# Kernel tuning notes

Hardware: AMD Instinct MI355X
Metric: run time of the kernel (lower is better)

Reference implementation:

```python
import jax, jax.numpy as jnp
import numpy as np

D_MODEL = 1024
N_HEADS = 16
D_V = D_MODEL // N_HEADS  # 64; o_proj maps d_model -> d_v (quirk of the source)
B, S = 4, 2048


def setup_inputs() -> dict:
    key = jax.random.key(0)
    ks = jax.random.split(key, 5)
    scale = 1.0 / np.sqrt(D_MODEL)
    return {
        "in_features": jax.random.normal(ks[0], (B, S, D_MODEL), dtype=jnp.float32),
        "Wq": jax.random.normal(ks[1], (D_MODEL, D_MODEL), dtype=jnp.float32) * scale,
        "Wk": jax.random.normal(ks[2], (D_MODEL, D_MODEL), dtype=jnp.float32) * scale,
        "Wv": jax.random.normal(ks[3], (D_MODEL, D_MODEL), dtype=jnp.float32) * scale,
        "Wo": jax.random.normal(ks[4], (D_V, D_MODEL), dtype=jnp.float32) * scale,
    }


def reference(in_features, Wq, Wk, Wv, Wo):
    # Linear(in, out): y = x @ W^T, no bias. NOTE: source never splits heads;
    # attention runs single-head over the full d_model dims.
    Q = jnp.einsum('bsd,ed->bse', in_features, Wq)  # [B,S,D]
    K = jnp.einsum('bsd,ed->bse', in_features, Wk)
    V = jnp.einsum('bsd,ed->bse', in_features, Wv)

    scores = jnp.einsum('bqd,bkd->bqk', Q, K)       # [B,S,S]
    causal = jnp.tril(jnp.ones((S, S), dtype=bool))  # True = keep
    # source applies -inf mask BEFORE scaling (equivalent result)
    scores = jnp.where(causal[None, :, :], scores, -jnp.inf)
    scores = scores / jnp.sqrt(jnp.float32(D_MODEL))  # K.size(-1) == d_model
    attn = jax.nn.softmax(scores, axis=-1)
    ctx = jnp.einsum('bqk,bkd->bqd', attn, V)        # [B,S,D]
    return jnp.einsum('bsd,vd->bsv', ctx, Wo)        # [B,S,D_V]
```

## Files before the change

kernel.cpp:

```cpp
#include <hip/hip_runtime.h>
#include <math.h>

typedef unsigned short u16;
typedef unsigned int u32;
typedef __attribute__((ext_vector_type(8))) short short8;
typedef __attribute__((ext_vector_type(4))) short short4v;
typedef __attribute__((ext_vector_type(4))) float f32x4;

#define BB 4
#define SS 2048
#define DD 1024
#define DV 64
#define NYU 1152
#define BS (BB * SS)
#define SCALE (1.0f / 32.0f)

__device__ __forceinline__ u16 f2bf(float f) {
    u32 u = __builtin_bit_cast(u32, f);
    u32 r = u + 0x7fffu + ((u >> 16) & 1u);
    return (u16)(r >> 16);
}
__device__ __forceinline__ float bf2f(u16 b) {
    return __builtin_bit_cast(float, (u32)b << 16);
}
__device__ __forceinline__ void storeC(float* p, float v) { *p = v; }
__device__ __forceinline__ void storeC(u16* p, float v) { *p = f2bf(v); }

__global__ __launch_bounds__(256) void prep(const float* __restrict__ x,
                                            const float* __restrict__ Wq,
                                            const float* __restrict__ Wk,
                                            const float* __restrict__ Wo,
                                            const float* __restrict__ Wv,
                                            u16* __restrict__ x16,
                                            u16* __restrict__ Wqt,
                                            u16* __restrict__ Wkt,
                                            float* __restrict__ wpart,
                                            float* __restrict__ out,
                                            float* __restrict__ Lacc) {
    __shared__ float smem[64 * 128];
    const int b = blockIdx.x;
    const int tid = threadIdx.x;
    if (b < 8192) {
        int i = b * 256 + tid;
        f32x4 v = ((const f32x4*)x)[i];
        short4v o;
        o.x = (short)f2bf(v.x); o.y = (short)f2bf(v.y);
        o.z = (short)f2bf(v.z); o.w = (short)f2bf(v.w);
        ((short4v*)x16)[i] = o;
    } else if (b < 8704) {
        const int bb = b - 8192;
        const float* src = (bb >> 8) ? Wk : Wq;
        u16* dst = (bb >> 8) ? Wkt : Wqt;
        const int rem = bb & 255;
        const int e0 = (rem >> 4) * 64, d0 = (rem & 15) * 64;
        u16* t = (u16*)smem;
        const int g = tid >> 6, lane = tid & 63;
        for (int r = g; r < 64; r += 4)
            t[r * 72 + lane] = f2bf(src[(size_t)(e0 + r) * DD + d0 + lane]);
        __syncthreads();
        for (int r = g; r < 64; r += 4)
            dst[(size_t)(d0 + r) * DD + e0 + lane] = t[lane * 72 + r];
    } else if (b < 8768) {
        const int bb = b - 8704;
        const int echunk = (bb & 7) * 128;
        const int kc = bb >> 3, kbase = kc * 128;
        for (int idx = tid; idx < 64 * 128; idx += 256)
            smem[idx] = Wo[(size_t)(idx >> 7) * DD + kbase + (idx & 127)];
        __syncthreads();
        const int eo = echunk + (tid & 31) * 4;
        const int ob = (tid >> 5) * 8;
        float acc[8][4] = {};
        for (int k = 0; k < 128; ++k) {
            f32x4 wv = *(const f32x4*)&Wv[(size_t)(kbase + k) * DD + eo];
#pragma unroll
            for (int oi = 0; oi < 8; ++oi) {
                float s = smem[(ob + oi) * 128 + k];
                acc[oi][0] += s * wv.x; acc[oi][1] += s * wv.y;
                acc[oi][2] += s * wv.z; acc[oi][3] += s * wv.w;
            }
        }
#pragma unroll
        for (int oi = 0; oi < 8; ++oi)
            *(f32x4*)&wpart[((size_t)kc * 64 + ob + oi) * DD + eo] =
                (f32x4){acc[oi][0], acc[oi][1], acc[oi][2], acc[oi][3]};
    } else if (b < 9280) {
        int i = (b - 8768) * 256 + tid;
        ((f32x4*)out)[i] = (f32x4){0.f, 0.f, 0.f, 0.f};
    } else {
        int i = (b - 9280) * 256 + tid;
        ((f32x4*)Lacc)[i] = (f32x4){0.f, 0.f, 0.f, 0.f};
    }
}

__global__ __launch_bounds__(256) void reduce_all(const float* __restrict__ Gpart,
                                                  const float* __restrict__ wpart,
                                                  u16* __restrict__ Wall2) {
    const int bx = blockIdx.x;
    const int e0 = threadIdx.x * 4;
    f32x4 s = (f32x4){0.f, 0.f, 0.f, 0.f};
    if (bx < 1024) {
#pragma unroll
        for (int kc = 0; kc < 4; ++kc)
            s += *(const f32x4*)&Gpart[(size_t)kc * DD * DD + (size_t)bx * DD + e0];
    } else {
#pragma unroll
        for (int kc = 0; kc < 8; ++kc)
            s += *(const f32x4*)&wpart[((size_t)kc * 64 + bx - 1024) * DD + e0];
    }
    short4v ov;
    ov.x = (short)f2bf(s.x); ov.y = (short)f2bf(s.y);
    ov.z = (short)f2bf(s.z); ov.w = (short)f2bf(s.w);
    *(short4v*)&Wall2[(size_t)bx * DD + e0] = ov;
}

template <int TM, int TN, int WM, int WN, typename OutT, int MODE>
__global__ __launch_bounds__(WM * WN * 64) void gemm_nt_mfma(
    const u16* __restrict__ A, const u16* __restrict__ B, OutT* __restrict__ C,
    int lda, int ldb, int ldc, int K, long sA, long sB, long sC,
    u16* __restrict__ Utp) {
    constexpr int NW = WM * WN;
    constexpr int CA = TM / 16;
    constexpr int CB = TN / 16;

    const int z = blockIdx.z;
    A += (size_t)z * sA;
    B += (size_t)z * sB;
    C += (size_t)z * sC;
    int m0, n0;
    if constexpr (MODE == 3) {
        const int b = blockIdx.x;
        const int r = b & 7, q = b >> 3;
        m0 = (r * 8 + q / 9) * TM;
        n0 = (q % 9) * TN;
    } else {
        m0 = blockIdx.y * TM;
        n0 = blockIdx.x * TN;
    }

    __shared__ u16 As[2][TM * 32];
    __shared__ u16 Bs[2][TN * 32];

    const int tid = threadIdx.x;
    const int w = tid >> 6, lane = tid & 63;
    const int wm = w / WN, wn = w % WN;
    const int lrow = lane >> 2;
    const int lcolsw = (((lane & 3) ^ ((lrow >> 1) & 3)) << 3);
    const int m16 = lane & 15;
    const int khg = lane >> 4;
    const int rdo = ((khg ^ ((m16 >> 1) & 3)) << 3);

    f32x4 acc[4][4];
#pragma unroll
    for (int i = 0; i < 4; ++i)
#pragma unroll
        for (int j = 0; j < 4; ++j) acc[i][j] = (f32x4){0.f, 0.f, 0.f, 0.f};

    auto stage = [&](int t, int bufi) {
        const int k0 = t * 32;
        for (int c = w; c < CA; c += NW) {
            const u16* g = A + (size_t)(m0 + c * 16 + lrow) * lda + k0 + lcolsw;
            __builtin_amdgcn_global_load_lds(
                (const __attribute__((address_space(1))) void*)g,
                (__attribute__((address_space(3))) void*)(&As[bufi][c * 512]), 16, 0, 0);
        }
        for (int c = w; c < CB; c += NW) {
            const u16* g = B + (size_t)(n0 + c * 16 + lrow) * ldb + k0 + lcolsw;
            __builtin_amdgcn_global_load_lds(
                (const __attribute__((address_space(1))) void*)g,
                (__attribute__((address_space(3))) void*)(&Bs[bufi][c * 512]), 16, 0, 0);
        }
    };

    const int nk = K >> 5;
    stage(0, 0);
    int cur = 0;
    for (int t = 0; t < nk; ++t) {
        asm volatile("s_waitcnt vmcnt(0)" ::: "memory");
        __syncthreads();
        if (t + 1 < nk) stage(t + 1, cur ^ 1);

        short8 a[4], b[4];
#pragma unroll
        for (int i = 0; i < 4; ++i)
            a[i] = *(const short8*)&As[cur][(wm * 64 + i * 16 + m16) * 32 + rdo];
#pragma unroll
        for (int j = 0; j < 4; ++j)
            b[j] = *(const short8*)&Bs[cur][(wn * 64 + j * 16 + m16) * 32 + rdo];
#pragma unroll
        for (int i = 0; i < 4; ++i)
#pragma unroll
            for (int j = 0; j < 4; ++j)
                acc[i][j] = __builtin_amdgcn_mfma_f32_16x16x32_bf16(a[i], b[j], acc[i][j], 0, 0, 0);
        cur ^= 1;
    }

    const int crow0 = m0 + wm * 64 + (lane >> 4) * 4;
    const int ccol0 = n0 + wn * 64 + m16;
#pragma unroll
    for (int i = 0; i < 4; ++i)
#pragma unroll
        for (int j = 0; j < 4; ++j)
#pragma unroll
            for (int r = 0; r < 4; ++r) {
                const float v = acc[i][j][r];
                storeC(&C[(size_t)(crow0 + i * 16 + r) * ldc + ccol0 + j * 16], v);
                if constexpr (MODE == 3) {
                    if (n0 == 1024 && wn == 0)
                        Utp[(size_t)(ccol0 + j * 16 - 1024) * BS + crow0 + i * 16 + r] = f2bf(v);
                }
            }
}

__global__ __launch_bounds__(256) void scores_pv(const u16* __restrict__ YU,
                                                 const u16* __restrict__ x16,
                                                 const u16* __restrict__ Ut,
                                                 float* __restrict__ out,
                                                 float* __restrict__ Lacc) {
    const int b = blockIdx.x;
    const int r8 = b & 7;
    const int z = r8 >> 1;
    const int t = 2 * (b >> 3) + (r8 & 1);
    int y = (int)((sqrtf(8.f * t + 1.f) - 1.f) * 0.5f);
    while ((y + 1) * (y + 2) / 2 <= t) ++y;
    while (y * (y + 1) / 2 > t) --y;
    const int m0 = y * 128;
    const int n0 = (t - y * (y + 1) / 2) * 128;

    const u16* A = YU + (size_t)z * SS * NYU;
    const u16* B = x16 + (size_t)z * SS * DD;

    __shared__ union ShU {
        struct { u16 As[2][128 * 32]; u16 Bs[2][128 * 32]; } s;
        u16 Ps[128 * 136];
    } sh;

    const int tid = threadIdx.x;
    const int w = tid >> 6, lane = tid & 63;
    const int wm = w >> 1, wn = w & 1;
    const int lrow = lane >> 2;
    const int lcolsw = (((lane & 3) ^ ((lrow >> 1) & 3)) << 3);
    const int m16 = lane & 15;
    const int kh = (lane >> 4) * 8;
    const int rdo = (((lane >> 4) ^ ((m16 >> 1) & 3)) << 3);

    f32x4 acc[4][4];
#pragma unroll
    for (int i = 0; i < 4; ++i)
#pragma unroll
        for (int j = 0; j < 4; ++j) acc[i][j] = (f32x4){0.f, 0.f, 0.f, 0.f};

    auto stage = [&](int tt, int bufi) {
        const int k0 = tt * 32;
        for (int c = w; c < 8; c += 4) {
            const u16* g = A + (size_t)(m0 + c * 16 + lrow) * NYU + k0 + lcolsw;
            __builtin_amdgcn_global_load_lds(
                (const __attribute__((address_space(1))) void*)g,
                (__attribute__((address_space(3))) void*)(&sh.s.As[bufi][c * 512]), 16, 0, 0);
        }
        for (int c = w; c < 8; c += 4) {
            const u16* g = B + (size_t)(n0 + c * 16 + lrow) * DD + k0 + lcolsw;
            __builtin_amdgcn_global_load_lds(
                (const __attribute__((address_space(1))) void*)g,
                (__attribute__((address_space(3))) void*)(&sh.s.Bs[bufi][c * 512]), 16, 0, 0);
        }
    };

    stage(0, 0);
    int cur = 0;
    for (int tt = 0; tt < 32; ++tt) {
        asm volatile("s_waitcnt vmcnt(0)" ::: "memory");
        __syncthreads();
        if (tt + 1 < 32) stage(tt + 1, cur ^ 1);

        short8 a[4], bb[4];
#pragma unroll
        for (int i = 0; i < 4; ++i)
            a[i] = *(const short8*)&sh.s.As[cur][(wm * 64 + i * 16 + m16) * 32 + rdo];
#pragma unroll
        for (int j = 0; j < 4; ++j)
            bb[j] = *(const short8*)&sh.s.Bs[cur][(wn * 64 + j * 16 + m16) * 32 + rdo];
#pragma unroll
        for (int i = 0; i < 4; ++i)
#pragma unroll
            for (int j = 0; j < 4; ++j)
                acc[i][j] = __builtin_amdgcn_mfma_f32_16x16x32_bf16(a[i], bb[j], acc[i][j], 0, 0, 0);
        cur ^= 1;
    }
    __syncthreads();

    const int rl0 = wm * 64 + (lane >> 4) * 4;
    const int cl0 = wn * 64 + m16;
#pragma unroll
    for (int i = 0; i < 4; ++i)
#pragma unroll
        for (int j = 0; j < 4; ++j)
#pragma unroll
            for (int r = 0; r < 4; ++r) {
                const int rl = rl0 + i * 16 + r;
                const int cl = cl0 + j * 16;
                float p = __expf(acc[i][j][r] * SCALE);
                sh.Ps[rl * 136 + cl] = (n0 + cl <= m0 + rl) ? f2bf(p) : (u16)0;
            }
    __syncthreads();

    short8 ones8;
#pragma unroll
    for (int e = 0; e < 8; ++e) ones8[e] = (short)0x3F80;

    const u16* Utz = Ut + (size_t)z * SS + n0;
    f32x4 accO[2][4], accL[2];
#pragma unroll
    for (int i = 0; i < 2; ++i) {
        accL[i] = (f32x4){0.f, 0.f, 0.f, 0.f};
#pragma unroll
        for (int j = 0; j < 4; ++j) accO[i][j] = (f32x4){0.f, 0.f, 0.f, 0.f};
    }
#pragma unroll
    for (int ks = 0; ks < 4; ++ks) {
        const int k0 = ks * 32;
        short8 a[2], bb[4];
#pragma unroll
        for (int i = 0; i < 2; ++i)
            a[i] = *(const short8*)&sh.Ps[(w * 32 + i * 16 + m16) * 136 + k0 + kh];
#pragma unroll
        for (int j = 0; j < 4; ++j)
            bb[j] = *(const short8*)&Utz[(size_t)(j * 16 + m16) * BS + k0 + kh];
#pragma unroll
        for (int i = 0; i < 2; ++i) {
#pragma unroll
            for (int j = 0; j < 4; ++j)
                accO[i][j] = __builtin_amdgcn_mfma_f32_16x16x32_bf16(a[i], bb[j], accO[i][j], 0, 0, 0);
            accL[i] = __builtin_amdgcn_mfma_f32_16x16x32_bf16(a[i], ones8, accL[i], 0, 0, 0);
        }
    }

    float* Oz = out + (size_t)z * SS * DV;
    float* Lz = Lacc + (size_t)z * SS;
    const int wrow = m0 + w * 32 + (lane >> 4) * 4;
#pragma unroll
    for (int i = 0; i < 2; ++i) {
#pragma unroll
        for (int j = 0; j < 4; ++j)
#pragma unroll
            for (int r = 0; r < 4; ++r)
                atomicAdd(&Oz[(size_t)(wrow + i * 16 + r) * DV + j * 16 + m16],
                          accO[i][j][r]);
        if (m16 == 0)
#pragma unroll
            for (int r = 0; r < 4; ++r)
                atomicAdd(&Lz[wrow + i * 16 + r], accL[i][r]);
    }
}

__global__ __launch_bounds__(256) void normalize(float* __restrict__ out,
                                                 const float* __restrict__ Lacc) {
    int i = blockIdx.x * 256 + threadIdx.x;
    f32x4 v = ((f32x4*)out)[i];
    const float inv = 1.f / Lacc[(i * 4) >> 6];
    v.x *= inv; v.y *= inv; v.z *= inv; v.w *= inv;
    ((f32x4*)out)[i] = v;
}

extern "C" void kernel_launch(void* const* d_in, const int* in_sizes, int n_in,
                              void* d_out, int out_size, void* d_ws, size_t ws_size,
                              hipStream_t stream) {
    const float* x  = (const float*)d_in[0];
    const float* Wq = (const float*)d_in[1];
    const float* Wk = (const float*)d_in[2];
    const float* Wv = (const float*)d_in[3];
    const float* Wo = (const float*)d_in[4];
    float* out = (float*)d_out;

    u16* x16   = (u16*)d_ws;
    u16* Wqt16 = x16 + (size_t)BB * SS * DD;
    u16* Wkt16 = Wqt16 + (size_t)DD * DD;
    u16* Wall2 = Wkt16 + (size_t)DD * DD;
    u16* YU    = Wall2 + (size_t)NYU * DD;
    u16* Ut    = YU + (size_t)BB * SS * NYU;
    float* wpart = (float*)(Ut + (size_t)DV * BS);
    float* Lacc  = wpart + (size_t)8 * 64 * DD;
    float* Gpart = (float*)YU;

    prep<<<dim3(9288), 256, 0, stream>>>(x, Wq, Wk, Wo, Wv, x16, Wqt16, Wkt16,
                                         wpart, out, Lacc);

    gemm_nt_mfma<128, 128, 2, 2, float, 0><<<dim3(8, 8, 4), 256, 0, stream>>>(
        Wkt16, Wqt16, Gpart, DD, DD, DD, 256, 256, 256, (long)DD * DD, nullptr);

    reduce_all<<<dim3(1088), 256, 0, stream>>>(Gpart, wpart, Wall2);

    gemm_nt_mfma<128, 128, 2, 2, u16, 3><<<dim3(576), 256, 0, stream>>>(
        x16, Wall2, YU, DD, DD, NYU, DD, 0, 0, 0, Ut);

    scores_pv<<<dim3(544), 256, 0, stream>>>(YU, x16, Ut, out, Lacc);

    normalize<<<dim3(out_size / 4 / 256), 256, 0, stream>>>(out, Lacc);
}
```

Before: 200.2 us.

## Triple-buffer GEMM K-loop with partial vmcnt waits and smaller Gram tiles

The GEMM and scores kernels move from double to triple buffering in LDS. Loads for tile t+2 are issued before computing tile t, and the wait only drains older loads (vmcnt(LPT)), leaving one barrier per iteration. The GEMM template is generalized to any tile size, and the Wq/Wk Gram GEMM moves to 64x64 tiles to launch more blocks. The prep kernel is also reordered so the long Wv·Wo blocks are scheduled first. This raises LDS usage, which may lower occupancy, and the scores kernel's union grows to fit three buffers.

```diff
diff --git a/kernel.cpp b/kernel.cpp
--- a/kernel.cpp
+++ b/kernel.cpp
@@ -25,6 +25,17 @@
 }
 __device__ __forceinline__ void storeC(float* p, float v) { *p = v; }
 __device__ __forceinline__ void storeC(u16* p, float v) { *p = f2bf(v); }
+
+template <int N>
+__device__ __forceinline__ void wait_vm() {
+    if constexpr (N == 0) asm volatile("s_waitcnt vmcnt(0)" ::: "memory");
+    else if constexpr (N == 1) asm volatile("s_waitcnt vmcnt(1)" ::: "memory");
+    else if constexpr (N == 2) asm volatile("s_waitcnt vmcnt(2)" ::: "memory");
+    else if constexpr (N == 3) asm volatile("s_waitcnt vmcnt(3)" ::: "memory");
+    else if constexpr (N == 4) asm volatile("s_waitcnt vmcnt(4)" ::: "memory");
+    else if constexpr (N == 6) asm volatile("s_waitcnt vmcnt(6)" ::: "memory");
+    else if constexpr (N == 8) asm volatile("s_waitcnt vmcnt(8)" ::: "memory");
+}
 
 __global__ __launch_bounds__(256) void prep(const float* __restrict__ x,
                                             const float* __restrict__ Wq,
@@ -40,15 +51,31 @@
     __shared__ float smem[64 * 128];
     const int b = blockIdx.x;
     const int tid = threadIdx.x;
-    if (b < 8192) {
-        int i = b * 256 + tid;
-        f32x4 v = ((const f32x4*)x)[i];
-        short4v o;
-        o.x = (short)f2bf(v.x); o.y = (short)f2bf(v.y);
-        o.z = (short)f2bf(v.z); o.w = (short)f2bf(v.w);
-        ((short4v*)x16)[i] = o;
-    } else if (b < 8704) {
-        const int bb = b - 8192;
+    if (b < 64) {
+        const int bb = b;
+        const int echunk = (bb & 7) * 128;
+        const int kc = bb >> 3, kbase = kc * 128;
+        for (int idx = tid; idx < 64 * 128; idx += 256)
+            smem[idx] = Wo[(size_t)(idx >> 7) * DD + kbase + (idx & 127)];
+        __syncthreads();
+        const int eo = echunk + (tid & 31) * 4;
+        const int ob = (tid >> 5) * 8;
+        float acc[8][4] = {};
+        for (int k = 0; k < 128; ++k) {
+            f32x4 wv = *(const f32x4*)&Wv[(size_t)(kbase + k) * DD + eo];
+#pragma unroll
+            for (int oi = 0; oi < 8; ++oi) {
+                float s = smem[(ob + oi) * 128 + k];
+                acc[oi][0] += s * wv.x; acc[oi][1] += s * wv.y;
+                acc[oi][2] += s * wv.z; acc[oi][3] += s * wv.w;
+            }
+        }
+#pragma unroll
+        for (int oi = 0; oi < 8; ++oi)
+            *(f32x4*)&wpart[((size_t)kc * 64 + ob + oi) * DD + eo] =
+                (f32x4){acc[oi][0], acc[oi][1], acc[oi][2], acc[oi][3]};
+    } else if (b < 576) {
+        const int bb = b - 64;
         const float* src = (bb >> 8) ? Wk : Wq;
         u16* dst = (bb >> 8) ? Wkt : Wqt;
         const int rem = bb & 255;
@@ -61,28 +88,12 @@
         for (int r = g; r < 64; r += 4)
             dst[(size_t)(d0 + r) * DD + e0 + lane] = t[lane * 72 + r];
     } else if (b < 8768) {
-        const int bb = b - 8704;
-        const int echunk = (bb & 7) * 128;
-        const int kc = bb >> 3, kbase = kc * 128;
-        for (int idx = tid; idx < 64 * 128; idx += 256)
-            smem[idx] = Wo[(size_t)(idx >> 7) * DD + kbase + (idx & 127)];
-        __syncthreads();
-        const int eo = echunk + (tid & 31) * 4;
-        const int ob = (tid >> 5) * 8;
-        float acc[8][4] = {};
-        for (int k = 0; k < 128; ++k) {
-            f32x4 wv = *(const f32x4*)&Wv[(size_t)(kbase + k) * DD + eo];
-#pragma unroll
-            for (int oi = 0; oi < 8; ++oi) {
-                float s = smem[(ob + oi) * 128 + k];
-                acc[oi][0] += s * wv.x; acc[oi][1] += s * wv.y;
-                acc[oi][2] += s * wv.z; acc[oi][3] += s * wv.w;
-            }
-        }
-#pragma unroll
-        for (int oi = 0; oi < 8; ++oi)
-            *(f32x4*)&wpart[((size_t)kc * 64 + ob + oi) * DD + eo] =
-                (f32x4){acc[oi][0], acc[oi][1], acc[oi][2], acc[oi][3]};
+        int i = (b - 576) * 256 + tid;
+        f32x4 v = ((const f32x4*)x)[i];
+        short4v o;
+        o.x = (short)f2bf(v.x); o.y = (short)f2bf(v.y);
+        o.z = (short)f2bf(v.z); o.w = (short)f2bf(v.w);
+        ((short4v*)x16)[i] = o;
     } else if (b < 9280) {
         int i = (b - 8768) * 256 + tid;
         ((f32x4*)out)[i] = (f32x4){0.f, 0.f, 0.f, 0.f};
@@ -121,6 +132,11 @@
     constexpr int NW = WM * WN;
     constexpr int CA = TM / 16;
     constexpr int CB = TN / 16;
+    constexpr int RT = TM / WM;
+    constexpr int CT = TN / WN;
+    constexpr int AI = RT / 16;
+    constexpr int AJ = CT / 16;
+    constexpr int LPT = CA / NW + CB / NW;
 
     const int z = blockIdx.z;
     A += (size_t)z * sA;
@@ -130,15 +146,16 @@
     if constexpr (MODE == 3) {
         const int b = blockIdx.x;
         const int r = b & 7, q = b >> 3;
-        m0 = (r * 8 + q / 9) * TM;
+        constexpr int RPX = 8192 / TM / 8;
+        m0 = (r * RPX + q / 9) * TM;
         n0 = (q % 9) * TN;
     } else {
         m0 = blockIdx.y * TM;
         n0 = blockIdx.x * TN;
     }
 
-    __shared__ u16 As[2][TM * 32];
-    __shared__ u16 Bs[2][TN * 32];
+    __shared__ u16 As[3][TM * 32];
+    __shared__ u16 Bs[3][TN * 32];
 
     const int tid = threadIdx.x;
     const int w = tid >> 6, lane = tid & 63;
@@ -146,14 +163,13 @@
     const int lrow = lane >> 2;
     const int lcolsw = (((lane & 3) ^ ((lrow >> 1) & 3)) << 3);
     const int m16 = lane & 15;
-    const int khg = lane >> 4;
-    const int rdo = ((khg ^ ((m16 >> 1) & 3)) << 3);
-
-    f32x4 acc[4][4];
-#pragma unroll
-    for (int i = 0; i < 4; ++i)
-#pragma unroll
-        for (int j = 0; j < 4; ++j) acc[i][j] = (f32x4){0.f, 0.f, 0.f, 0.f};
+    const int rdo = (((lane >> 4) ^ ((m16 >> 1) & 3)) << 3);
+
+    f32x4 acc[AI][AJ];
+#pragma unroll
+    for (int i = 0; i < AI; ++i)
+#pragma unroll
+        for (int j = 0; j < AJ; ++j) acc[i][j] = (f32x4){0.f, 0.f, 0.f, 0.f};
 
     auto stage = [&](int t, int bufi) {
         const int k0 = t * 32;
@@ -173,33 +189,38 @@
 
     const int nk = K >> 5;
     stage(0, 0);
-    int cur = 0;
+    if (nk > 1) { stage(1, 1); wait_vm<LPT>(); } else { wait_vm<0>(); }
+    __syncthreads();
+
+    int rb = 0, sb = 2;
     for (int t = 0; t < nk; ++t) {
-        asm volatile("s_waitcnt vmcnt(0)" ::: "memory");
-        __syncthreads();
-        if (t + 1 < nk) stage(t + 1, cur ^ 1);
-
-        short8 a[4], b[4];
-#pragma unroll
-        for (int i = 0; i < 4; ++i)
-            a[i] = *(const short8*)&As[cur][(wm * 64 + i * 16 + m16) * 32 + rdo];
-#pragma unroll
-        for (int j = 0; j < 4; ++j)
-            b[j] = *(const short8*)&Bs[cur][(wn * 64 + j * 16 + m16) * 32 + rdo];
-#pragma unroll
-        for (int i = 0; i < 4; ++i)
-#pragma unroll
-            for (int j = 0; j < 4; ++j)
+        if (t + 2 < nk) stage(t + 2, sb);
+
+        short8 a[AI], b[AJ];
+#pragma unroll
+        for (int i = 0; i < AI; ++i)
+            a[i] = *(const short8*)&As[rb][(wm * RT + i * 16 + m16) * 32 + rdo];
+#pragma unroll
+        for (int j = 0; j < AJ; ++j)
+            b[j] = *(const short8*)&Bs[rb][(wn * CT + j * 16 + m16) * 32 + rdo];
+#pragma unroll
+        for (int i = 0; i < AI; ++i)
+#pragma unroll
+            for (int j = 0; j < AJ; ++j)
                 acc[i][j] = __builtin_amdgcn_mfma_f32_16x16x32_bf16(a[i], b[j], acc[i][j], 0, 0, 0);
-        cur ^= 1;
-    }
-
-    const int crow0 = m0 + wm * 64 + (lane >> 4) * 4;
-    const int ccol0 = n0 + wn * 64 + m16;
-#pragma unroll
-    for (int i = 0; i < 4; ++i)
-#pragma unroll
-        for (int j = 0; j < 4; ++j)
+
+        if (t + 2 < nk) { wait_vm<LPT>(); __syncthreads(); }
+        else if (t + 1 < nk) { wait_vm<0>(); __syncthreads(); }
+        rb = (rb == 2) ? 0 : rb + 1;
+        sb = (sb == 2) ? 0 : sb + 1;
+    }
+
+    const int crow0 = m0 + wm * RT + (lane >> 4) * 4;
+    const int ccol0 = n0 + wn * CT + m16;
+#pragma unroll
+    for (int i = 0; i < AI; ++i)
+#pragma unroll
+        for (int j = 0; j < AJ; ++j)
 #pragma unroll
             for (int r = 0; r < 4; ++r) {
                 const float v = acc[i][j][r];
@@ -230,7 +251,7 @@
     const u16* B = x16 + (size_t)z * SS * DD;
 
     __shared__ union ShU {
-        struct { u16 As[2][128 * 32]; u16 Bs[2][128 * 32]; } s;
+        struct { u16 As[3][128 * 32]; u16 Bs[3][128 * 32]; } s;
         u16 Ps[128 * 136];
     } sh;
 
@@ -266,25 +287,31 @@
     };
 
     stage(0, 0);
-    int cur = 0;
+    stage(1, 1);
+    wait_vm<4>();
+    __syncthreads();
+
+    int rb = 0, sb = 2;
     for (int tt = 0; tt < 32; ++tt) {
-        asm volatile("s_waitcnt vmcnt(0)" ::: "memory");
-        __syncthreads();
-        if (tt + 1 < 32) stage(tt + 1, cur ^ 1);
+        if (tt + 2 < 32) stage(tt + 2, sb);
 
         short8 a[4], bb[4];
 #pragma unroll
         for (int i = 0; i < 4; ++i)
-            a[i] = *(const short8*)&sh.s.As[cur][(wm * 64 + i * 16 + m16) * 32 + rdo];
+            a[i] = *(const short8*)&sh.s.As[rb][(wm * 64 + i * 16 + m16) * 32 + rdo];
 #pragma unroll
         for (int j = 0; j < 4; ++j)
-            bb[j] = *(const short8*)&sh.s.Bs[cur][(wn * 64 + j * 16 + m16) * 32 + rdo];
+            bb[j] = *(const short8*)&sh.s.Bs[rb][(wn * 64 + j * 16 + m16) * 32 + rdo];
 #pragma unroll
         for (int i = 0; i < 4; ++i)
 #pragma unroll
             for (int j = 0; j < 4; ++j)
                 acc[i][j] = __builtin_amdgcn_mfma_f32_16x16x32_bf16(a[i], bb[j], acc[i][j], 0, 0, 0);
-        cur ^= 1;
+
+        if (tt + 2 < 32) { wait_vm<4>(); __syncthreads(); }
+        else if (tt + 1 < 32) { wait_vm<0>(); __syncthreads(); }
+        rb = (rb == 2) ? 0 : rb + 1;
+        sb = (sb == 2) ? 0 : sb + 1;
     }
     __syncthreads();
 
@@ -384,7 +411,7 @@
     prep<<<dim3(9288), 256, 0, stream>>>(x, Wq, Wk, Wo, Wv, x16, Wqt16, Wkt16,
                                          wpart, out, Lacc);
 
-    gemm_nt_mfma<128, 128, 2, 2, float, 0><<<dim3(8, 8, 4), 256, 0, stream>>>(
+    gemm_nt_mfma<64, 64, 2, 2, float, 0><<<dim3(16, 16, 4), 256, 0, stream>>>(
         Wkt16, Wqt16, Gpart, DD, DD, DD, 256, 256, 256, (long)DD * DD, nullptr);
 
     reduce_all<<<dim3(1088), 256, 0, stream>>>(Gpart, wpart, Wall2);
```

New measurement: 193.1 us. 3.6% less time.

## Replace atomics with per-tile partials, MFMA weight products, restructure GEMM pipeline sync

Applied to the files above, without the earlier changes.

scores_pv now writes each tile's partial output and row-sum into its own slot, and normalize reduces those slots per row. This removes the fp32 atomicAdds and the zero-fill passes over out and Lacc. The Wo·Wv product moves from a scalar fp32 loop in prep to a bf16 MFMA kernel that also computes the split-K Wk^T·Wq Gram partials in 64x64 tiles. Partials are stored in bf16, which halves reduce traffic but loses some precision. The double-buffered GEMM loops now issue the next stage before waiting, giving slightly more load/compute overlap, and the template GEMM is split into specialized kernels.

```diff
diff --git a/kernel.cpp b/kernel.cpp
--- a/kernel.cpp
+++ b/kernel.cpp
@@ -14,6 +14,8 @@
 #define NYU 1152
 #define BS (BB * SS)
 #define SCALE (1.0f / 32.0f)
+#define NTILE 136
+#define NSLOT (BB * NTILE)
 
 __device__ __forceinline__ u16 f2bf(float f) {
     u32 u = __builtin_bit_cast(u32, f);
@@ -23,131 +25,191 @@
 __device__ __forceinline__ float bf2f(u16 b) {
     return __builtin_bit_cast(float, (u32)b << 16);
 }
-__device__ __forceinline__ void storeC(float* p, float v) { *p = v; }
-__device__ __forceinline__ void storeC(u16* p, float v) { *p = f2bf(v); }
 
 __global__ __launch_bounds__(256) void prep(const float* __restrict__ x,
                                             const float* __restrict__ Wq,
                                             const float* __restrict__ Wk,
+                                            const float* __restrict__ Wv,
                                             const float* __restrict__ Wo,
-                                            const float* __restrict__ Wv,
                                             u16* __restrict__ x16,
                                             u16* __restrict__ Wqt,
                                             u16* __restrict__ Wkt,
-                                            float* __restrict__ wpart,
-                                            float* __restrict__ out,
-                                            float* __restrict__ Lacc) {
-    __shared__ float smem[64 * 128];
+                                            u16* __restrict__ Wvt,
+                                            u16* __restrict__ Wo16) {
+    __shared__ u16 t[64 * 72];
     const int b = blockIdx.x;
     const int tid = threadIdx.x;
-    if (b < 8192) {
-        int i = b * 256 + tid;
-        f32x4 v = ((const f32x4*)x)[i];
-        short4v o;
-        o.x = (short)f2bf(v.x); o.y = (short)f2bf(v.y);
-        o.z = (short)f2bf(v.z); o.w = (short)f2bf(v.w);
-        ((short4v*)x16)[i] = o;
-    } else if (b < 8704) {
-        const int bb = b - 8192;
-        const float* src = (bb >> 8) ? Wk : Wq;
-        u16* dst = (bb >> 8) ? Wkt : Wqt;
-        const int rem = bb & 255;
+    if (b < 768) {
+        const int sel = b >> 8;
+        const float* src = (sel == 0) ? Wq : (sel == 1) ? Wk : Wv;
+        u16* dst = (sel == 0) ? Wqt : (sel == 1) ? Wkt : Wvt;
+        const int rem = b & 255;
         const int e0 = (rem >> 4) * 64, d0 = (rem & 15) * 64;
-        u16* t = (u16*)smem;
         const int g = tid >> 6, lane = tid & 63;
         for (int r = g; r < 64; r += 4)
             t[r * 72 + lane] = f2bf(src[(size_t)(e0 + r) * DD + d0 + lane]);
         __syncthreads();
         for (int r = g; r < 64; r += 4)
             dst[(size_t)(d0 + r) * DD + e0 + lane] = t[lane * 72 + r];
-    } else if (b < 8768) {
-        const int bb = b - 8704;
-        const int echunk = (bb & 7) * 128;
-        const int kc = bb >> 3, kbase = kc * 128;
-        for (int idx = tid; idx < 64 * 128; idx += 256)
-            smem[idx] = Wo[(size_t)(idx >> 7) * DD + kbase + (idx & 127)];
-        __syncthreads();
-        const int eo = echunk + (tid & 31) * 4;
-        const int ob = (tid >> 5) * 8;
-        float acc[8][4] = {};
-        for (int k = 0; k < 128; ++k) {
-            f32x4 wv = *(const f32x4*)&Wv[(size_t)(kbase + k) * DD + eo];
-#pragma unroll
-            for (int oi = 0; oi < 8; ++oi) {
-                float s = smem[(ob + oi) * 128 + k];
-                acc[oi][0] += s * wv.x; acc[oi][1] += s * wv.y;
-                acc[oi][2] += s * wv.z; acc[oi][3] += s * wv.w;
-            }
-        }
-#pragma unroll
-        for (int oi = 0; oi < 8; ++oi)
-            *(f32x4*)&wpart[((size_t)kc * 64 + ob + oi) * DD + eo] =
-                (f32x4){acc[oi][0], acc[oi][1], acc[oi][2], acc[oi][3]};
-    } else if (b < 9280) {
-        int i = (b - 8768) * 256 + tid;
-        ((f32x4*)out)[i] = (f32x4){0.f, 0.f, 0.f, 0.f};
+    } else if (b < 784) {
+#pragma unroll
+        for (int j = 0; j < 4; ++j) {
+            int i = (b - 768) * 1024 + j * 256 + tid;
+            f32x4 v = ((const f32x4*)Wo)[i];
+            short4v o;
+            o.x = (short)f2bf(v.x); o.y = (short)f2bf(v.y);
+            o.z = (short)f2bf(v.z); o.w = (short)f2bf(v.w);
+            ((short4v*)Wo16)[i] = o;
+        }
     } else {
-        int i = (b - 9280) * 256 + tid;
-        ((f32x4*)Lacc)[i] = (f32x4){0.f, 0.f, 0.f, 0.f};
-    }
-}
-
-__global__ __launch_bounds__(256) void reduce_all(const float* __restrict__ Gpart,
-                                                  const float* __restrict__ wpart,
+        int i = (b - 784) * 256 + tid;
+        f32x4 v = ((const f32x4*)x)[i];
+        short4v o;
+        o.x = (short)f2bf(v.x); o.y = (short)f2bf(v.y);
+        o.z = (short)f2bf(v.z); o.w = (short)f2bf(v.w);
+        ((short4v*)x16)[i] = o;
+    }
+}
+
+__global__ __launch_bounds__(256) void gt_wvo(const u16* __restrict__ Wkt,
+                                              const u16* __restrict__ Wqt,
+                                              const u16* __restrict__ Wo16,
+                                              const u16* __restrict__ Wvt,
+                                              u16* __restrict__ GpartH,
+                                              u16* __restrict__ WvoPartH) {
+    const int b = blockIdx.x;
+    const u16 *A, *B;
+    u16* C;
+    int m0, n0;
+    if (b < 1024) {
+        const int z = b >> 8, t = b & 255;
+        A = Wkt + z * 256;
+        B = Wqt + z * 256;
+        C = GpartH + (size_t)z * DD * DD;
+        m0 = (t >> 4) * 64;
+        n0 = (t & 15) * 64;
+    } else {
+        const int bb = b - 1024;
+        const int kc = bb >> 4, t = bb & 15;
+        A = Wo16 + kc * 256;
+        B = Wvt + kc * 256;
+        C = WvoPartH + (size_t)kc * DV * DD;
+        m0 = 0;
+        n0 = t * 64;
+    }
+
+    __shared__ u16 As[2][64 * 32];
+    __shared__ u16 Bs[2][64 * 32];
+
+    const int tid = threadIdx.x;
+    const int w = tid >> 6, lane = tid & 63;
+    const int wm = w >> 1, wn = w & 1;
+    const int lrow = lane >> 2;
+    const int lcolsw = (((lane & 3) ^ ((lrow >> 1) & 3)) << 3);
+    const int m16 = lane & 15;
+    const int rdo = (((lane >> 4) ^ ((m16 >> 1) & 3)) << 3);
+
+    f32x4 acc[2][2];
+#pragma unroll
+    for (int i = 0; i < 2; ++i)
+#pragma unroll
+        for (int j = 0; j < 2; ++j) acc[i][j] = (f32x4){0.f, 0.f, 0.f, 0.f};
+
+    auto stage = [&](int t_, int bufi) {
+        const int k0 = t_ * 32;
+        {
+            const u16* g = A + (size_t)(m0 + w * 16 + lrow) * DD + k0 + lcolsw;
+            __builtin_amdgcn_global_load_lds(
+                (const __attribute__((address_space(1))) void*)g,
+                (__attribute__((address_space(3))) void*)(&As[bufi][w * 512]), 16, 0, 0);
+        }
+        {
+            const u16* g = B + (size_t)(n0 + w * 16 + lrow) * DD + k0 + lcolsw;
+            __builtin_amdgcn_global_load_lds(
+                (const __attribute__((address_space(1))) void*)g,
+                (__attribute__((address_space(3))) void*)(&Bs[bufi][w * 512]), 16, 0, 0);
+        }
+    };
+
+    stage(0, 0);
+    asm volatile("s_waitcnt vmcnt(0)" ::: "memory");
+    __syncthreads();
+
+    int cur = 0;
+    for (int t_ = 0; t_ < 8; ++t_) {
+        if (t_ + 1 < 8) stage(t_ + 1, cur ^ 1);
+
+        short8 a[2], bb[2];
+#pragma unroll
+        for (int i = 0; i < 2; ++i)
+            a[i] = *(const short8*)&As[cur][(wm * 32 + i * 16 + m16) * 32 + rdo];
+#pragma unroll
+        for (int j = 0; j < 2; ++j)
+            bb[j] = *(const short8*)&Bs[cur][(wn * 32 + j * 16 + m16) * 32 + rdo];
+#pragma unroll
+        for (int i = 0; i < 2; ++i)
+#pragma unroll
+            for (int j = 0; j < 2; ++j)
+                acc[i][j] = __builtin_amdgcn_mfma_f32_16x16x32_bf16(a[i], bb[j], acc[i][j], 0, 0, 0);
+
+        if (t_ + 1 < 8) {
+            asm volatile("s_waitcnt vmcnt(0)" ::: "memory");
+            __syncthreads();
+        }
+        cur ^= 1;
+    }
+
+    const int crow0 = m0 + wm * 32 + (lane >> 4) * 4;
+    const int ccol0 = n0 + wn * 32 + m16;
+#pragma unroll
+    for (int i = 0; i < 2; ++i)
+#pragma unroll
+        for (int j = 0; j < 2; ++j)
+#pragma unroll
+            for (int r = 0; r < 4; ++r)
+                C[(size_t)(crow0 + i * 16 + r) * DD + ccol0 + j * 16] = f2bf(acc[i][j][r]);
+}
+
+__global__ __launch_bounds__(256) void reduce_all(const u16* __restrict__ GpartH,
+                                                  const u16* __restrict__ WvoPartH,
                                                   u16* __restrict__ Wall2) {
     const int bx = blockIdx.x;
     const int e0 = threadIdx.x * 4;
-    f32x4 s = (f32x4){0.f, 0.f, 0.f, 0.f};
-    if (bx < 1024) {
-#pragma unroll
-        for (int kc = 0; kc < 4; ++kc)
-            s += *(const f32x4*)&Gpart[(size_t)kc * DD * DD + (size_t)bx * DD + e0];
-    } else {
-#pragma unroll
-        for (int kc = 0; kc < 8; ++kc)
-            s += *(const f32x4*)&wpart[((size_t)kc * 64 + bx - 1024) * DD + e0];
+    float s0 = 0.f, s1 = 0.f, s2 = 0.f, s3 = 0.f;
+#pragma unroll
+    for (int kc = 0; kc < 4; ++kc) {
+        const u16* src = (bx < 1024)
+                             ? &GpartH[(size_t)kc * DD * DD + (size_t)bx * DD + e0]
+                             : &WvoPartH[(size_t)kc * DV * DD + (size_t)(bx - 1024) * DD + e0];
+        short4v v = *(const short4v*)src;
+        s0 += bf2f((u16)v.x); s1 += bf2f((u16)v.y);
+        s2 += bf2f((u16)v.z); s3 += bf2f((u16)v.w);
     }
     short4v ov;
-    ov.x = (short)f2bf(s.x); ov.y = (short)f2bf(s.y);
-    ov.z = (short)f2bf(s.z); ov.w = (short)f2bf(s.w);
+    ov.x = (short)f2bf(s0); ov.y = (short)f2bf(s1);
+    ov.z = (short)f2bf(s2); ov.w = (short)f2bf(s3);
     *(short4v*)&Wall2[(size_t)bx * DD + e0] = ov;
 }
 
-template <int TM, int TN, int WM, int WN, typename OutT, int MODE>
-__global__ __launch_bounds__(WM * WN * 64) void gemm_nt_mfma(
-    const u16* __restrict__ A, const u16* __restrict__ B, OutT* __restrict__ C,
-    int lda, int ldb, int ldc, int K, long sA, long sB, long sC,
-    u16* __restrict__ Utp) {
-    constexpr int NW = WM * WN;
-    constexpr int CA = TM / 16;
-    constexpr int CB = TN / 16;
-
-    const int z = blockIdx.z;
-    A += (size_t)z * sA;
-    B += (size_t)z * sB;
-    C += (size_t)z * sC;
-    int m0, n0;
-    if constexpr (MODE == 3) {
-        const int b = blockIdx.x;
-        const int r = b & 7, q = b >> 3;
-        m0 = (r * 8 + q / 9) * TM;
-        n0 = (q % 9) * TN;
-    } else {
-        m0 = blockIdx.y * TM;
-        n0 = blockIdx.x * TN;
-    }
-
-    __shared__ u16 As[2][TM * 32];
-    __shared__ u16 Bs[2][TN * 32];
+__global__ __launch_bounds__(256) void yu_gemm(const u16* __restrict__ x16,
+                                               const u16* __restrict__ Wall2,
+                                               u16* __restrict__ YU,
+                                               u16* __restrict__ Ut) {
+    const int b = blockIdx.x;
+    const int r = b & 7, q = b >> 3;
+    const int m0 = (r * 8 + q / 9) * 128;
+    const int n0 = (q % 9) * 128;
+
+    __shared__ u16 As[2][128 * 32];
+    __shared__ u16 Bs[2][128 * 32];
 
     const int tid = threadIdx.x;
     const int w = tid >> 6, lane = tid & 63;
-    const int wm = w / WN, wn = w % WN;
+    const int wm = w >> 1, wn = w & 1;
     const int lrow = lane >> 2;
     const int lcolsw = (((lane & 3) ^ ((lrow >> 1) & 3)) << 3);
     const int m16 = lane & 15;
-    const int khg = lane >> 4;
-    const int rdo = ((khg ^ ((m16 >> 1) & 3)) << 3);
+    const int rdo = (((lane >> 4) ^ ((m16 >> 1) & 3)) << 3);
 
     f32x4 acc[4][4];
 #pragma unroll
@@ -157,40 +219,45 @@
 
     auto stage = [&](int t, int bufi) {
         const int k0 = t * 32;
-        for (int c = w; c < CA; c += NW) {
-            const u16* g = A + (size_t)(m0 + c * 16 + lrow) * lda + k0 + lcolsw;
+        for (int c = w; c < 8; c += 4) {
+            const u16* g = x16 + (size_t)(m0 + c * 16 + lrow) * DD + k0 + lcolsw;
             __builtin_amdgcn_global_load_lds(
                 (const __attribute__((address_space(1))) void*)g,
                 (__attribute__((address_space(3))) void*)(&As[bufi][c * 512]), 16, 0, 0);
         }
-        for (int c = w; c < CB; c += NW) {
-            const u16* g = B + (size_t)(n0 + c * 16 + lrow) * ldb + k0 + lcolsw;
+        for (int c = w; c < 8; c += 4) {
+            const u16* g = Wall2 + (size_t)(n0 + c * 16 + lrow) * DD + k0 + lcolsw;
             __builtin_amdgcn_global_load_lds(
                 (const __attribute__((address_space(1))) void*)g,
                 (__attribute__((address_space(3))) void*)(&Bs[bufi][c * 512]), 16, 0, 0);
         }
     };
 
-    const int nk = K >> 5;
     stage(0, 0);
+    asm volatile("s_waitcnt vmcnt(0)" ::: "memory");
+    __syncthreads();
+
     int cur = 0;
-    for (int t = 0; t < nk; ++t) {
-        asm volatile("s_waitcnt vmcnt(0)" ::: "memory");
-        __syncthreads();
-        if (t + 1 < nk) stage(t + 1, cur ^ 1);
-
-        short8 a[4], b[4];
+    for (int t = 0; t < 32; ++t) {
+        if (t + 1 < 32) stage(t + 1, cur ^ 1);
+
+        short8 a[4], bb[4];
 #pragma unroll
         for (int i = 0; i < 4; ++i)
             a[i] = *(const short8*)&As[cur][(wm * 64 + i * 16 + m16) * 32 + rdo];
 #pragma unroll
         for (int j = 0; j < 4; ++j)
-            b[j] = *(const short8*)&Bs[cur][(wn * 64 + j * 16 + m16) * 32 + rdo];
+            bb[j] = *(const short8*)&Bs[cur][(wn * 64 + j * 16 + m16) * 32 + rdo];
 #pragma unroll
         for (int i = 0; i < 4; ++i)
 #pragma unroll
             for (int j = 0; j < 4; ++j)
-                acc[i][j] = __builtin_amdgcn_mfma_f32_16x16x32_bf16(a[i], b[j], acc[i][j], 0, 0, 0);
+                acc[i][j] = __builtin_amdgcn_mfma_f32_16x16x32_bf16(a[i], bb[j], acc[i][j], 0, 0, 0);
+
+        if (t + 1 < 32) {
+            asm volatile("s_waitcnt vmcnt(0)" ::: "memory");
+            __syncthreads();
+        }
         cur ^= 1;
     }
 
@@ -203,19 +270,17 @@
 #pragma unroll
             for (int r = 0; r < 4; ++r) {
                 const float v = acc[i][j][r];
-                storeC(&C[(size_t)(crow0 + i * 16 + r) * ldc + ccol0 + j * 16], v);
-                if constexpr (MODE == 3) {
-                    if (n0 == 1024 && wn == 0)
-                        Utp[(size_t)(ccol0 + j * 16 - 1024) * BS + crow0 + i * 16 + r] = f2bf(v);
-                }
+                YU[(size_t)(crow0 + i * 16 + r) * NYU + ccol0 + j * 16] = f2bf(v);
+                if (n0 == 1024 && wn == 0)
+                    Ut[(size_t)(ccol0 + j * 16 - 1024) * BS + crow0 + i * 16 + r] = f2bf(v);
             }
 }
 
 __global__ __launch_bounds__(256) void scores_pv(const u16* __restrict__ YU,
                                                  const u16* __restrict__ x16,
                                                  const u16* __restrict__ Ut,
-                                                 float* __restrict__ out,
-                                                 float* __restrict__ Lacc) {
+                                                 float* __restrict__ Opart,
+                                                 float* __restrict__ Lpart) {
     const int b = blockIdx.x;
     const int r8 = b & 7;
     const int z = r8 >> 1;
@@ -225,6 +290,7 @@
     while (y * (y + 1) / 2 > t) --y;
     const int m0 = y * 128;
     const int n0 = (t - y * (y + 1) / 2) * 128;
+    const int tglob = z * NTILE + t;
 
     const u16* A = YU + (size_t)z * SS * NYU;
     const u16* B = x16 + (size_t)z * SS * DD;
@@ -266,10 +332,11 @@
     };
 
     stage(0, 0);
+    asm volatile("s_waitcnt vmcnt(0)" ::: "memory");
+    __syncthreads();
+
     int cur = 0;
     for (int tt = 0; tt < 32; ++tt) {
-        asm volatile("s_waitcnt vmcnt(0)" ::: "memory");
-        __syncthreads();
         if (tt + 1 < 32) stage(tt + 1, cur ^ 1);
 
         short8 a[4], bb[4];
@@ -284,6 +351,11 @@
 #pragma unroll
             for (int j = 0; j < 4; ++j)
                 acc[i][j] = __builtin_amdgcn_mfma_f32_16x16x32_bf16(a[i], bb[j], acc[i][j], 0, 0, 0);
+
+        if (tt + 1 < 32) {
+            asm volatile("s_waitcnt vmcnt(0)" ::: "memory");
+            __syncthreads();
+        }
         cur ^= 1;
     }
     __syncthreads();
@@ -334,31 +406,44 @@
         }
     }
 
-    float* Oz = out + (size_t)z * SS * DV;
-    float* Lz = Lacc + (size_t)z * SS;
-    const int wrow = m0 + w * 32 + (lane >> 4) * 4;
+    float* Op = Opart + (size_t)tglob * (128 * 64);
+    float* Lp = Lpart + (size_t)tglob * 128;
+    const int lr0 = w * 32 + (lane >> 4) * 4;
 #pragma unroll
     for (int i = 0; i < 2; ++i) {
 #pragma unroll
         for (int j = 0; j < 4; ++j)
 #pragma unroll
             for (int r = 0; r < 4; ++r)
-                atomicAdd(&Oz[(size_t)(wrow + i * 16 + r) * DV + j * 16 + m16],
-                          accO[i][j][r]);
+                Op[(size_t)(lr0 + i * 16 + r) * DV + j * 16 + m16] = accO[i][j][r];
         if (m16 == 0)
 #pragma unroll
             for (int r = 0; r < 4; ++r)
-                atomicAdd(&Lz[wrow + i * 16 + r], accL[i][r]);
+                Lp[lr0 + i * 16 + r] = accL[i][r];
     }
 }
 
 __global__ __launch_bounds__(256) void normalize(float* __restrict__ out,
-                                                 const float* __restrict__ Lacc) {
-    int i = blockIdx.x * 256 + threadIdx.x;
-    f32x4 v = ((f32x4*)out)[i];
-    const float inv = 1.f / Lacc[(i * 4) >> 6];
-    v.x *= inv; v.y *= inv; v.z *= inv; v.w *= inv;
-    ((f32x4*)out)[i] = v;
+                                                 const float* __restrict__ Opart,
+                                                 const float* __restrict__ Lpart) {
+    const int i = blockIdx.x * 256 + threadIdx.x;
+    const int row = i >> 4;
+    const int z = row >> 11, s = row & 2047;
+    const int y = s >> 7, lr = s & 127;
+    const int base = z * NTILE + y * (y + 1) / 2;
+    const int nc = y + 1;
+    const int col4 = (i & 15) * 4;
+
+    f32x4 acc = (f32x4){0.f, 0.f, 0.f, 0.f};
+    float L = 0.f;
+    for (int c = 0; c < nc; ++c) {
+        const int slot = base + c;
+        acc += *(const f32x4*)&Opart[(size_t)slot * (128 * 64) + (size_t)lr * 64 + col4];
+        L += Lpart[(size_t)slot * 128 + lr];
+    }
+    const float inv = 1.f / L;
+    acc.x *= inv; acc.y *= inv; acc.z *= inv; acc.w *= inv;
+    ((f32x4*)out)[i] = acc;
 }
 
 extern "C" void kernel_launch(void* const* d_in, const int* in_sizes, int n_in,
@@ -372,27 +457,27 @@
     float* out = (float*)d_out;
 
     u16* x16   = (u16*)d_ws;
-    u16* Wqt16 = x16 + (size_t)BB * SS * DD;
-    u16* Wkt16 = Wqt16 + (size_t)DD * DD;
-    u16* Wall2 = Wkt16 + (size_t)DD * DD;
+    u16* Wqt   = x16 + (size_t)BB * SS * DD;
+    u16* Wkt   = Wqt + (size_t)DD * DD;
+    u16* Wvt   = Wkt + (size_t)DD * DD;
+    u16* Wo16  = Wvt + (size_t)DD * DD;
+    u16* Wall2 = Wo16 + (size_t)DV * DD;
     u16* YU    = Wall2 + (size_t)NYU * DD;
     u16* Ut    = YU + (size_t)BB * SS * NYU;
-    float* wpart = (float*)(Ut + (size_t)DV * BS);
-    float* Lacc  = wpart + (size_t)8 * 64 * DD;
-    float* Gpart = (float*)YU;
-
-    prep<<<dim3(9288), 256, 0, stream>>>(x, Wq, Wk, Wo, Wv, x16, Wqt16, Wkt16,
-                                         wpart, out, Lacc);
-
-    gemm_nt_mfma<128, 128, 2, 2, float, 0><<<dim3(8, 8, 4), 256, 0, stream>>>(
-        Wkt16, Wqt16, Gpart, DD, DD, DD, 256, 256, 256, (long)DD * DD, nullptr);
-
-    reduce_all<<<dim3(1088), 256, 0, stream>>>(Gpart, wpart, Wall2);
-
-    gemm_nt_mfma<128, 128, 2, 2, u16, 3><<<dim3(576), 256, 0, stream>>>(
-        x16, Wall2, YU, DD, DD, NYU, DD, 0, 0, 0, Ut);
-
-    scores_pv<<<dim3(544), 256, 0, stream>>>(YU, x16, Ut, out, Lacc);
-
-    normalize<<<dim3(out_size / 4 / 256), 256, 0, stream>>>(out, Lacc);
-}
+    float* Opart = (float*)(Ut + (size_t)DV * BS);
+    float* Lpart = Opart + (size_t)NSLOT * 128 * DV;
+    u16* GpartH   = YU;
+    u16* WvoPartH = GpartH + (size_t)4 * DD * DD;
+
+    prep<<<dim3(8976), 256, 0, stream>>>(x, Wq, Wk, Wv, Wo, x16, Wqt, Wkt, Wvt, Wo16);
+
+    gt_wvo<<<dim3(1088), 256, 0, stream>>>(Wkt, Wqt, Wo16, Wvt, GpartH, WvoPartH);
+
+    reduce_all<<<dim3(1088), 256, 0, stream>>>(GpartH, WvoPartH, Wall2);
+
+    yu_gemm<<<dim3(576), 256, 0, stream>>>(x16, Wall2, YU, Ut);
+
+    scores_pv<<<dim3(544), 256, 0, stream>>>(YU, x16, Ut, Opart, Lpart);
+
+    normalize<<<dim3(out_size / 4 / 256), 256, 0, stream>>>(out, Opart, Lpart);
+}
```

After: 192.3 us. -3.9%, faster.
